# Kernel tuning notes

Measured on AMD Instinct MI355X. Metric: run time of the kernel, lower is better.

Reference implementation:

```python
import jax, jax.numpy as jnp
import numpy as np

IMG_DIM = 256
AUD_DIM = 256
N_HEADS = 8


def _linear_params(key, fan_in, fan_out):
    k1, k2 = jax.random.split(key)
    lim = 1.0 / np.sqrt(fan_in)
    W = jax.random.uniform(k1, (fan_in, fan_out), minval=-lim, maxval=lim, dtype=jnp.float32)
    b = jax.random.uniform(k2, (fan_out,), minval=-lim, maxval=lim, dtype=jnp.float32)
    return W, b


def setup_inputs() -> dict:
    key = jax.random.key(0)
    ks = jax.random.split(key, 16)
    B, Nv, Na = 16, 1024, 512
    inp = {
        "image_feat": jax.random.normal(ks[0], (B, Nv, IMG_DIM), dtype=jnp.float32),
        "audio_feat": jax.random.normal(ks[1], (B, Na, AUD_DIM), dtype=jnp.float32),
    }
    inp["Wq_i"], inp["bq_i"] = _linear_params(ks[2], IMG_DIM, IMG_DIM)
    inp["Wk_i"], inp["bk_i"] = _linear_params(ks[3], IMG_DIM, IMG_DIM)
    inp["Wv_i"], inp["bv_i"] = _linear_params(ks[4], IMG_DIM, IMG_DIM)
    inp["Wo_i"], inp["bo_i"] = _linear_params(ks[5], AUD_DIM, IMG_DIM)  # out_proj_image
    inp["Wq_a"], inp["bq_a"] = _linear_params(ks[6], AUD_DIM, AUD_DIM)
    inp["Wk_a"], inp["bk_a"] = _linear_params(ks[7], AUD_DIM, AUD_DIM)
    inp["Wv_a"], inp["bv_a"] = _linear_params(ks[8], AUD_DIM, AUD_DIM)
    inp["Wo_a"], inp["bo_a"] = _linear_params(ks[9], IMG_DIM, AUD_DIM)  # out_proj_audio
    inp["Wc1_i"], inp["bc1_i"] = _linear_params(ks[10], IMG_DIM + 2, IMG_DIM)
    inp["Wc2_i"], inp["bc2_i"] = _linear_params(ks[11], IMG_DIM, N_HEADS)
    inp["Wc1_a"], inp["bc1_a"] = _linear_params(ks[12], AUD_DIM + 2, AUD_DIM)
    inp["Wc2_a"], inp["bc2_a"] = _linear_params(ks[13], AUD_DIM, N_HEADS)
    inp["Wg_i"], inp["bg_i"] = _linear_params(ks[14], IMG_DIM, IMG_DIM)
    inp["Wg_a"], inp["bg_a"] = _linear_params(ks[15], AUD_DIM, AUD_DIM)
    return inp


def _heads(x, W, b, H):
    # x: [B, N, C] -> [B, H, N, C//H]
    B, N, _ = x.shape
    y = x @ W + b
    return y.reshape(B, N, H, -1).transpose(0, 2, 1, 3)


def _fwd(image_feat, audio_feat,
         Wq_i, bq_i, Wk_i, bk_i, Wv_i, bv_i, Wo_i, bo_i,
         Wq_a, bq_a, Wk_a, bk_a, Wv_a, bv_a, Wo_a, bo_a,
         Wc1_i, bc1_i, Wc2_i, bc2_i, Wc1_a, bc1_a, Wc2_a, bc2_a,
         Wg_i, bg_i, Wg_a, bg_a):
    H = N_HEADS
    B, Nv, Ci = image_feat.shape
    _, Na, Ca = audio_feat.shape
    scale_img = (Ci // H) ** (-0.5)
    scale_aud = (Ca // H) ** (-0.5)

    tp_img = image_feat.mean(axis=1)  # [B, Ci]
    tp_aud = audio_feat.mean(axis=1)  # [B, Ca]
    spatial_cond = jnp.linalg.norm(image_feat, axis=-1).mean(axis=1, keepdims=True)  # [B,1]
    time_cond = jnp.linalg.norm(audio_feat, axis=-1).mean(axis=1, keepdims=True)     # [B,1]

    # --- audio queries attend over image keys/values ---
    Q_a = _heads(audio_feat, Wq_a, bq_a, H)   # [B,H,Na,d]
    K_i = _heads(image_feat, Wk_i, bk_i, H)   # [B,H,Nv,d]
    V_i = _heads(image_feat, Wv_i, bv_i, H)   # [B,H,Nv,d]
    cond_aud = jnp.concatenate([tp_aud, spatial_cond, time_cond], axis=-1)  # [B,Ca+2]
    bias_a = (jax.nn.relu(cond_aud @ Wc1_a + bc1_a) @ Wc2_a + bc2_a)        # [B,H]
    logits_a = jnp.einsum('bhqd,bhkd->bhqk', Q_a, K_i) * scale_aud + bias_a[:, :, None, None]
    attn_a = jax.nn.softmax(logits_a, axis=-1)
    fused_a = jnp.einsum('bhqk,bhkd->bhqd', attn_a, V_i)  # [B,H,Na,d]
    fused_a = fused_a.transpose(0, 2, 1, 3).reshape(B, Na, Ci)
    fused_a = fused_a @ Wo_a + bo_a                        # [B,Na,Ca]
    gate_a = jax.nn.sigmoid(tp_aud @ Wg_a + bg_a)[:, None, :]
    audio_out = gate_a * fused_a + (1.0 - gate_a) * audio_feat

    # --- image queries attend over UPDATED audio keys/values ---
    Q_i = _heads(image_feat, Wq_i, bq_i, H)   # [B,H,Nv,d]
    K_a = _heads(audio_out, Wk_a, bk_a, H)    # [B,H,Na,d]
    V_a = _heads(audio_out, Wv_a, bv_a, H)    # [B,H,Na,d]
    cond_img = jnp.concatenate([tp_img, spatial_cond, time_cond], axis=-1)  # [B,Ci+2]
    bias_i = (jax.nn.relu(cond_img @ Wc1_i + bc1_i) @ Wc2_i + bc2_i)        # [B,H]
    logits_i = jnp.einsum('bhqd,bhkd->bhqk', Q_i, K_a) * scale_img + bias_i[:, :, None, None]
    attn_i = jax.nn.softmax(logits_i, axis=-1)
    fused_i = jnp.einsum('bhqk,bhkd->bhqd', attn_i, V_a)  # [B,H,Nv,d]
    fused_i = fused_i.transpose(0, 2, 1, 3).reshape(B, Nv, Ca)
    fused_i = fused_i @ Wo_i + bo_i                        # [B,Nv,Ci]
    gate_i = jax.nn.sigmoid(tp_img @ Wg_i + bg_i)[:, None, :]
    image_out = gate_i * fused_i + (1.0 - gate_i) * image_feat

    return image_out, audio_out


def reference(image_feat, audio_feat,
              Wq_i, bq_i, Wk_i, bk_i, Wv_i, bv_i, Wo_i, bo_i,
              Wq_a, bq_a, Wk_a, bk_a, Wv_a, bv_a, Wo_a, bo_a,
              Wc1_i, bc1_i, Wc2_i, bc2_i, Wc1_a, bc1_a, Wc2_a, bc2_a,
              Wg_i, bg_i, Wg_a, bg_a):
    return _fwd(image_feat, audio_feat,
                Wq_i, bq_i, Wk_i, bk_i, Wv_i, bv_i, Wo_i, bo_i,
                Wq_a, bq_a, Wk_a, bk_a, Wv_a, bv_a, Wo_a, bo_a,
                Wc1_i, bc1_i, Wc2_i, bc2_i, Wc1_a, bc1_a, Wc2_a, bc2_a,
                Wg_i, bg_i, Wg_a, bg_a)
```

## Files before the change

### kernel.cpp

```cpp
#include <hip/hip_runtime.h>

#define C 256

typedef short s16x8 __attribute__((ext_vector_type(8)));
typedef float f32x4 __attribute__((ext_vector_type(4)));

#if __has_builtin(__builtin_amdgcn_exp2f)
#define EXP2F __builtin_amdgcn_exp2f
#else
#define EXP2F exp2f
#endif

__device__ __forceinline__ unsigned short f2b(float f) {
    unsigned u = __float_as_uint(f);
    unsigned r = (u + 0x7fffu + ((u >> 16) & 1u)) >> 16;
    return (unsigned short)r;
}

__device__ __forceinline__ unsigned pack2(float a, float b) {
    return __builtin_amdgcn_perm(__float_as_uint(b) + 0x8000u,
                                 __float_as_uint(a) + 0x8000u, 0x07060302u);
}

struct WPtrs { const float* src[8]; unsigned short* dst[8]; };

__device__ __forceinline__ void cast_mean_body(
    const float* __restrict__ x, unsigned short* __restrict__ y, float* __restrict__ part,
    int N, int nseg, int b, int seg, int tid) {
    __shared__ float red[4][C];
    int cg = tid & 63, rg = tid >> 6;
    int iters = nseg >> 2;
    const float* xp = x + ((size_t)b * N + (size_t)seg * nseg + rg) * C + cg * 4;
    unsigned short* yp = y + ((size_t)b * N + (size_t)seg * nseg + rg) * C + cg * 4;
    float s0 = 0.f, s1 = 0.f, s2 = 0.f, s3 = 0.f;
    for (int i = 0; i < iters; ++i) {
        float4 v = *(const float4*)(xp + (size_t)i * 4 * C);
        s0 += v.x; s1 += v.y; s2 += v.z; s3 += v.w;
        ushort4 o; o.x = f2b(v.x); o.y = f2b(v.y); o.z = f2b(v.z); o.w = f2b(v.w);
        *(ushort4*)(yp + (size_t)i * 4 * C) = o;
    }
    float4 s4 = {s0, s1, s2, s3};
    *(float4*)&red[rg][cg * 4] = s4;
    __syncthreads();
    float s = red[0][tid] + red[1][tid] + red[2][tid] + red[3][tid];
    part[(b * 8 + seg) * C + tid] = s;
}

__global__ void prep_kernel(const float* __restrict__ img, const float* __restrict__ aud,
                            unsigned short* __restrict__ R1, unsigned short* __restrict__ R4,
                            float* __restrict__ partI, float* __restrict__ partA, WPtrs wp) {
    int x = blockIdx.x, tid = threadIdx.x;
    if (x < 128) {
        cast_mean_body(img, R1, partI, 1024, 128, x >> 3, x & 7, tid);
    } else if (x < 256) {
        int id = x - 128;
        cast_mean_body(aud, R4, partA, 512, 64, id >> 3, id & 7, tid);
    } else {
        int id = x - 256;
        const float* W = wp.src[id >> 2];
        unsigned short* Wt = wp.dst[id >> 2];
        int n = (id & 3) * 64 + (tid & 63);
        int k0 = (tid >> 6) * 64;
#pragma unroll
        for (int kk = 0; kk < 64; kk += 4) {
            float a0 = W[(size_t)(k0 + kk + 0) * C + n];
            float a1 = W[(size_t)(k0 + kk + 1) * C + n];
            float a2 = W[(size_t)(k0 + kk + 2) * C + n];
            float a3 = W[(size_t)(k0 + kk + 3) * C + n];
            ushort4 o; o.x = f2b(a0); o.y = f2b(a1); o.z = f2b(a2); o.w = f2b(a3);
            *(ushort4*)(Wt + (size_t)n * C + k0 + kk) = o;
        }
    }
}

struct GDesc {
    const unsigned short* A;
    const unsigned short* Bt;
    const float* bias;
    unsigned short* Yh;
    int N;
    int start;
    int lnb;
    int bias_on_m;
    float oscale;
};
struct GArgs {
    GDesc d[4];
    int off1, off2, off3;
    int gemm_total;
    const float* partI; const float* partA;
    const float* WgI; const float* WgA;
    const float* bgI; const float* bgA;
    float* gI; float* gA;
    float invNv, invNa;
};

__global__ __launch_bounds__(256, 2) void gemm_multi(GArgs ga) {
    __shared__ unsigned short sA[128 * 40];
    __shared__ unsigned short sB[64 * 40];
    const int bid = blockIdx.x;
    const int tid = threadIdx.x;

    if (bid >= ga.gemm_total) {
        float* t = (float*)sA;
        int id = bid - ga.gemm_total;
        int b = id >> 1, which = id & 1;
        const float* part = which ? ga.partA : ga.partI;
        const float* Wg = which ? ga.WgA : ga.WgI;
        const float* bg = which ? ga.bgA : ga.bgI;
        float* g = which ? ga.gA : ga.gI;
        float invN = which ? ga.invNa : ga.invNv;
        float s = 0.f;
#pragma unroll
        for (int j = 0; j < 8; ++j) s += part[(b * 8 + j) * C + tid];
        t[tid] = s * invN;
        __syncthreads();
        float acc = bg[tid];
#pragma unroll 8
        for (int k = 0; k < C; ++k) acc += t[k] * Wg[k * C + tid];
        g[b * C + tid] = 1.f / (1.f + __expf(-acc));
        return;
    }

    const int j = (bid >= ga.off1) + (bid >= ga.off2) + (bid >= ga.off3);
    const GDesc d = ga.d[j];
    const int local = bid - d.start;
    const int bn = (local & ((1 << d.lnb) - 1)) * 64;
    const int bm = (local >> d.lnb) * 128;

    const int wave = tid >> 6, lane = tid & 63;
    const int quad = lane >> 4, l16 = lane & 15;
    const int ar0 = tid >> 2, ac0 = tid & 3;
    const int ar1 = (tid + 256) >> 2;
    const int br = tid >> 2, bc = tid & 3;

    f32x4 acc[2][4];
#pragma unroll
    for (int i = 0; i < 2; ++i)
#pragma unroll
        for (int k = 0; k < 4; ++k) acc[i][k] = (f32x4){0.f, 0.f, 0.f, 0.f};

    uint4 pa0 = *(const uint4*)(d.A + (size_t)(bm + ar0) * 256 + ac0 * 8);
    uint4 pa1 = *(const uint4*)(d.A + (size_t)(bm + ar1) * 256 + ac0 * 8);
    uint4 pb  = *(const uint4*)(d.Bt + (size_t)(bn + br) * 256 + bc * 8);

    for (int k0 = 0; k0 < 256; k0 += 32) {
        __syncthreads();
        *(uint4*)(sA + ar0 * 40 + ac0 * 8) = pa0;
        *(uint4*)(sA + ar1 * 40 + ac0 * 8) = pa1;
        *(uint4*)(sB + br * 40 + bc * 8) = pb;
        if (k0 < 224) {
            pa0 = *(const uint4*)(d.A + (size_t)(bm + ar0) * 256 + k0 + 32 + ac0 * 8);
            pa1 = *(const uint4*)(d.A + (size_t)(bm + ar1) * 256 + k0 + 32 + ac0 * 8);
            pb  = *(const uint4*)(d.Bt + (size_t)(bn + br) * 256 + k0 + 32 + bc * 8);
        }
        __syncthreads();
        s16x8 af[2], bf[4];
#pragma unroll
        for (int mt = 0; mt < 2; ++mt)
            af[mt] = *(const s16x8*)(sA + (wave * 32 + mt * 16 + l16) * 40 + quad * 8);
#pragma unroll
        for (int nt = 0; nt < 4; ++nt)
            bf[nt] = *(const s16x8*)(sB + (nt * 16 + l16) * 40 + quad * 8);
#pragma unroll
        for (int mt = 0; mt < 2; ++mt)
#pragma unroll
            for (int nt = 0; nt < 4; ++nt)
                acc[mt][nt] = __builtin_amdgcn_mfma_f32_16x16x32_bf16(af[mt], bf[nt], acc[mt][nt], 0, 0, 0);
    }

#pragma unroll
    for (int mt = 0; mt < 2; ++mt) {
#pragma unroll
        for (int nt = 0; nt < 4; ++nt) {
            int n = bn + nt * 16 + l16;
            float bias_n = d.bias_on_m ? 0.f : d.bias[n];
#pragma unroll
            for (int r = 0; r < 4; ++r) {
                int m = bm + wave * 32 + mt * 16 + quad * 4 + r;
                float y = acc[mt][nt][r] + (d.bias_on_m ? d.bias[m] : bias_n);
                d.Yh[(size_t)m * d.N + n] = f2b(y * d.oscale);
            }
        }
    }
}

template <bool STORE_BF16>
__global__ __launch_bounds__(256, 2) void gemm_out(
    const unsigned short* __restrict__ A, const unsigned short* __restrict__ Bt,
    const float* __restrict__ bias, float* __restrict__ Yf, unsigned short* __restrict__ Yh,
    int M, const float* __restrict__ gate, const float* __restrict__ resid, int rows_per_b) {
    __shared__ unsigned short sA[128 * 40];
    __shared__ unsigned short sB[64 * 40];
    const int tid = threadIdx.x;
    const int wave = tid >> 6, lane = tid & 63;
    const int quad = lane >> 4, l16 = lane & 15;
    const int bm = blockIdx.y * 128, bn = blockIdx.x * 64;
    const int ar0 = tid >> 2, ac0 = tid & 3;
    const int ar1 = (tid + 256) >> 2;
    const int br = tid >> 2, bc = tid & 3;

    f32x4 acc[2][4];
#pragma unroll
    for (int i = 0; i < 2; ++i)
#pragma unroll
        for (int k = 0; k < 4; ++k) acc[i][k] = (f32x4){0.f, 0.f, 0.f, 0.f};

    uint4 pa0 = *(const uint4*)(A + (size_t)(bm + ar0) * 256 + ac0 * 8);
    uint4 pa1 = *(const uint4*)(A + (size_t)(bm + ar1) * 256 + ac0 * 8);
    uint4 pb  = *(const uint4*)(Bt + (size_t)(bn + br) * 256 + bc * 8);

    for (int k0 = 0; k0 < 256; k0 += 32) {
        __syncthreads();
        *(uint4*)(sA + ar0 * 40 + ac0 * 8) = pa0;
        *(uint4*)(sA + ar1 * 40 + ac0 * 8) = pa1;
        *(uint4*)(sB + br * 40 + bc * 8) = pb;
        if (k0 < 224) {
            pa0 = *(const uint4*)(A + (size_t)(bm + ar0) * 256 + k0 + 32 + ac0 * 8);
            pa1 = *(const uint4*)(A + (size_t)(bm + ar1) * 256 + k0 + 32 + ac0 * 8);
            pb  = *(const uint4*)(Bt + (size_t)(bn + br) * 256 + k0 + 32 + bc * 8);
        }
        __syncthreads();
        s16x8 af[2], bf[4];
#pragma unroll
        for (int mt = 0; mt < 2; ++mt)
            af[mt] = *(const s16x8*)(sA + (wave * 32 + mt * 16 + l16) * 40 + quad * 8);
#pragma unroll
        for (int nt = 0; nt < 4; ++nt)
            bf[nt] = *(const s16x8*)(sB + (nt * 16 + l16) * 40 + quad * 8);
#pragma unroll
        for (int mt = 0; mt < 2; ++mt)
#pragma unroll
            for (int nt = 0; nt < 4; ++nt)
                acc[mt][nt] = __builtin_amdgcn_mfma_f32_16x16x32_bf16(af[mt], bf[nt], acc[mt][nt], 0, 0, 0);
    }

    const int b = bm / rows_per_b;
#pragma unroll
    for (int mt = 0; mt < 2; ++mt) {
#pragma unroll
        for (int nt = 0; nt < 4; ++nt) {
            int n = bn + nt * 16 + l16;
            float bias_n = bias[n];
            float g = gate[b * C + n];
#pragma unroll
            for (int r = 0; r < 4; ++r) {
                int m = bm + wave * 32 + mt * 16 + quad * 4 + r;
                float y = acc[mt][nt][r] + bias_n;
                float rv = resid[(size_t)m * C + n];
                y = g * y + (1.f - g) * rv;
                Yf[(size_t)m * C + n] = y;
                if (STORE_BF16) Yh[(size_t)m * C + n] = f2b(y);
            }
        }
    }
}

template <int Q2>
__global__ __launch_bounds__(256) void attn_mfma(
    const unsigned short* __restrict__ Q, const unsigned short* __restrict__ K,
    const unsigned short* __restrict__ Vt, unsigned short* __restrict__ O,
    int Nq, int Nk, int vtStride, int lnxb) {
    __shared__ unsigned short sK[64 * 40];
    __shared__ unsigned short sVt[32 * 72];
    __shared__ unsigned short sP[4][Q2][16 * 40];
    const int tid = threadIdx.x;
    const int wave = tid >> 6, lane = tid & 63;
    const int quad = lane >> 4, l16 = lane & 15;
    const int id = blockIdx.x;
    const int slot = id >> 3;
    const int bh = (id & 7) + 8 * (slot >> lnxb);
    const int xb = slot & ((1 << lnxb) - 1);
    const int b = bh >> 3, h = bh & 7;
    const int q0 = xb * (64 * Q2) + wave * (16 * Q2);

    s16x8 qf[Q2];
    f32x4 oacc[Q2][2];
    float rs[Q2];
#pragma unroll
    for (int q = 0; q < Q2; ++q) {
        qf[q] = *(const s16x8*)(Q + ((size_t)b * Nq + q0 + q * 16 + l16) * 256 + h * 32 + quad * 8);
        oacc[q][0] = (f32x4){0.f, 0.f, 0.f, 0.f};
        oacc[q][1] = (f32x4){0.f, 0.f, 0.f, 0.f};
        rs[q] = 0.f;
    }

    const int kr = tid >> 2, kc = tid & 3;
    const int vr = tid >> 3, vc = tid & 7;
    const unsigned short* Kb = K + (size_t)b * Nk * 256 + h * 32;
    const unsigned short* Vb = Vt + (size_t)(h * 32 + vr) * vtStride + (size_t)b * Nk;

    uint4 ka = *(const uint4*)(Kb + (size_t)kr * 256 + kc * 8);
    uint4 va = *(const uint4*)(Vb + vc * 8);
    const int n1 = (64 < Nk) ? 64 : 0;
    uint4 kb = *(const uint4*)(Kb + (size_t)(n1 + kr) * 256 + kc * 8);
    uint4 vb = *(const uint4*)(Vb + n1 + vc * 8);

    for (int k0 = 0; k0 < Nk; k0 += 64) {
        __syncthreads();
        *(uint4*)(sK + kr * 40 + kc * 8) = ka;
        *(uint4*)(sVt + vr * 72 + vc * 8) = va;
        ka = kb; va = vb;
        int np = k0 + 128; if (np >= Nk) np = Nk - 64;
        kb = *(const uint4*)(Kb + (size_t)(np + kr) * 256 + kc * 8);
        vb = *(const uint4*)(Vb + np + vc * 8);
        __syncthreads();

#pragma unroll
        for (int kt = 0; kt < 4; ++kt) {
            s16x8 kf = *(const s16x8*)(sK + (kt * 16 + l16) * 40 + quad * 8);
#pragma unroll
            for (int q = 0; q < Q2; ++q) {
                f32x4 z = (f32x4){0.f, 0.f, 0.f, 0.f};
                f32x4 st = __builtin_amdgcn_mfma_f32_16x16x32_bf16(kf, qf[q], z, 0, 0, 0);
                float p0 = EXP2F(st[0]), p1 = EXP2F(st[1]);
                float p2 = EXP2F(st[2]), p3 = EXP2F(st[3]);
                rs[q] += (p0 + p1) + (p2 + p3);
                uint2 pk;
                pk.x = pack2(p0, p1);
                pk.y = pack2(p2, p3);
                *(uint2*)(&sP[wave][q][0] + l16 * 40 + kt * 16 + quad * 4) = pk;
            }
        }
#pragma unroll
        for (int kg = 0; kg < 2; ++kg) {
            s16x8 vf0 = *(const s16x8*)(sVt + l16 * 72 + kg * 32 + quad * 8);
            s16x8 vf1 = *(const s16x8*)(sVt + (16 + l16) * 72 + kg * 32 + quad * 8);
#pragma unroll
            for (int q = 0; q < Q2; ++q) {
                s16x8 pf = *(const s16x8*)(&sP[wave][q][0] + l16 * 40 + kg * 32 + quad * 8);
                oacc[q][0] = __builtin_amdgcn_mfma_f32_16x16x32_bf16(pf, vf0, oacc[q][0], 0, 0, 0);
                oacc[q][1] = __builtin_amdgcn_mfma_f32_16x16x32_bf16(pf, vf1, oacc[q][1], 0, 0, 0);
            }
        }
    }

#pragma unroll
    for (int q = 0; q < Q2; ++q) {
        float r = rs[q];
        r += __shfl_xor(r, 16, 64);
        r += __shfl_xor(r, 32, 64);
        float inv = 1.f / r;
#pragma unroll
        for (int rr = 0; rr < 4; ++rr) {
            float iq = __shfl(inv, quad * 4 + rr, 64);
#pragma unroll
            for (int dh = 0; dh < 2; ++dh)
                O[((size_t)b * Nq + q0 + q * 16 + quad * 4 + rr) * 256 + h * 32 + dh * 16 + l16] =
                    f2b(oacc[q][dh][rr] * iq);
        }
    }
}

extern "C" void kernel_launch(void* const* d_in, const int* in_sizes, int n_in,
                              void* d_out, int out_size, void* d_ws, size_t ws_size,
                              hipStream_t stream) {
    (void)in_sizes; (void)n_in; (void)out_size; (void)ws_size;
    const float* img  = (const float*)d_in[0];
    const float* aud  = (const float*)d_in[1];
    const float* Wq_i = (const float*)d_in[2];  const float* bq_i = (const float*)d_in[3];
    const float* Wk_i = (const float*)d_in[4];  const float* bk_i = (const float*)d_in[5];
    const float* Wv_i = (const float*)d_in[6];  const float* bv_i = (const float*)d_in[7];
    const float* Wo_i = (const float*)d_in[8];  const float* bo_i = (const float*)d_in[9];
    const float* Wq_a = (const float*)d_in[10]; const float* bq_a = (const float*)d_in[11];
    const float* Wk_a = (const float*)d_in[12]; const float* bk_a = (const float*)d_in[13];
    const float* Wv_a = (const float*)d_in[14]; const float* bv_a = (const float*)d_in[15];
    const float* Wo_a = (const float*)d_in[16]; const float* bo_a = (const float*)d_in[17];
    const float* Wg_i = (const float*)d_in[26]; const float* bg_i = (const float*)d_in[27];
    const float* Wg_a = (const float*)d_in[28]; const float* bg_a = (const float*)d_in[29];

    const int B = 16, Nv = 1024, Na = 512;
    const int Mi = B * Nv, Ma = B * Na;
    const size_t MiC = (size_t)Mi * C;
    const size_t MaC = (size_t)Ma * C;

    float* out_img = (float*)d_out;
    float* out_aud = out_img + MiC;

    unsigned short* wsu = (unsigned short*)d_ws;
    unsigned short* R1 = wsu;
    unsigned short* R2 = R1 + MiC;
    unsigned short* R3 = R2 + MiC;
    unsigned short* R8 = R3 + MiC;
    unsigned short* R4 = R8 + MiC;
    unsigned short* R5 = R4 + MaC;
    unsigned short* R6 = R5 + MaC;
    unsigned short* R7 = R6 + MaC;
    unsigned short* wt = R7 + MaC;
    float* fws   = (float*)(wt + 8 * 65536);
    float* partI = fws;
    float* partA = partI + B * 8 * C;
    float* gI    = partA + B * 8 * C;
    float* gA    = gI + B * C;

    unsigned short* wtQa = wt + 0 * 65536;
    unsigned short* wtKi = wt + 1 * 65536;
    unsigned short* wtVi = wt + 2 * 65536;
    unsigned short* wtOa = wt + 3 * 65536;
    unsigned short* wtKa = wt + 4 * 65536;
    unsigned short* wtVa = wt + 5 * 65536;
    unsigned short* wtQi = wt + 6 * 65536;
    unsigned short* wtOi = wt + 7 * 65536;

    const float qs = 0.17677669529663687f * 1.4426950408889634f;
    dim3 blk(256);

    WPtrs wp;
    wp.src[0] = Wq_a; wp.dst[0] = wtQa;
    wp.src[1] = Wk_i; wp.dst[1] = wtKi;
    wp.src[2] = Wv_i; wp.dst[2] = wtVi;
    wp.src[3] = Wo_a; wp.dst[3] = wtOa;
    wp.src[4] = Wk_a; wp.dst[4] = wtKa;
    wp.src[5] = Wv_a; wp.dst[5] = wtVa;
    wp.src[6] = Wq_i; wp.dst[6] = wtQi;
    wp.src[7] = Wo_i; wp.dst[7] = wtOi;
    prep_kernel<<<288, blk, 0, stream>>>(img, aud, R1, R4, partI, partA, wp);

    GArgs g1 = {};
    g1.d[0] = {R4,   wtQa, bq_a, R5, 256,   0,    2, 0, qs };
    g1.d[1] = {R1,   wtKi, bk_i, R2, 256,   256,  2, 0, 1.f};
    g1.d[2] = {wtVi, R1,   bv_i, R3, 16384, 768,  8, 1, 1.f};
    g1.d[3] = {R1,   wtQi, bq_i, R8, 256,   1280, 2, 0, qs };
    g1.off1 = 256; g1.off2 = 768; g1.off3 = 1280; g1.gemm_total = 1792;
    g1.partI = partI; g1.partA = partA;
    g1.WgI = Wg_i; g1.WgA = Wg_a; g1.bgI = bg_i; g1.bgA = bg_a;
    g1.gI = gI; g1.gA = gA; g1.invNv = 1.f / Nv; g1.invNa = 1.f / Na;
    gemm_multi<<<1792 + 32, blk, 0, stream>>>(g1);

    attn_mfma<2><<<128 * (Na / 128), blk, 0, stream>>>(R5, R2, R3, R6, Na, Nv, Mi, 2);

    gemm_out<true><<<dim3(4, Ma / 128), blk, 0, stream>>>(R6, wtOa, bo_a, out_aud, R7, Ma, gA, aud, Na);

    GArgs g2 = {};
    g2.d[0] = {R7,   wtKa, bk_a, R5, 256,  0,   2, 0, 1.f};
    g2.d[1] = {wtVa, R7,   bv_a, R6, 8192, 256, 7, 1, 1.f};
    g2.off1 = 256; g2.off2 = 512; g2.off3 = 512; g2.gemm_total = 512;
    gemm_multi<<<512, blk, 0, stream>>>(g2);

    attn_mfma<2><<<128 * (Nv / 128), blk, 0, stream>>>(R8, R5, R6, R2, Nv, Na, Ma, 3);

    gemm_out<false><<<dim3(4, Mi / 128), blk, 0, stream>>>(R2, wtOi, bo_i, out_img, nullptr, Mi, gI, img, Nv);
}
```

Measured before the change: 243.9 us.

## Double GEMM K-tile to 64 and interleave attention P-compute with PV per key group

Both GEMM kernels now stage 64-wide K slices in shared memory (row stride 72) with four A and two B vector loads per thread. This halves the number of k-iterations and barrier pairs, at the cost of more LDS and more prefetch registers. The attention kernel now computes softmax probabilities for one 32-key group and immediately runs the PV MFMAs on that group. This lets the per-wave P scratch hold only 32 columns and shortens the gap between producing and consuming P.

New measurement: 319.0 us. 30.8% more time.

```diff
diff --git a/kernel.cpp b/kernel.cpp
--- a/kernel.cpp
+++ b/kernel.cpp
@@ -96,8 +96,8 @@
 };
 
 __global__ __launch_bounds__(256, 2) void gemm_multi(GArgs ga) {
-    __shared__ unsigned short sA[128 * 40];
-    __shared__ unsigned short sB[64 * 40];
+    __shared__ unsigned short sA[128 * 72];
+    __shared__ unsigned short sB[64 * 72];
     const int bid = blockIdx.x;
     const int tid = threadIdx.x;
 
@@ -130,9 +130,11 @@
 
     const int wave = tid >> 6, lane = tid & 63;
     const int quad = lane >> 4, l16 = lane & 15;
-    const int ar0 = tid >> 2, ac0 = tid & 3;
-    const int ar1 = (tid + 256) >> 2;
-    const int br = tid >> 2, bc = tid & 3;
+    int arw[4], acg[4], brw[2], bcg[2];
+#pragma unroll
+    for (int s = 0; s < 4; ++s) { int slot = tid + s * 256; arw[s] = slot >> 3; acg[s] = slot & 7; }
+#pragma unroll
+    for (int s = 0; s < 2; ++s) { int slot = tid + s * 256; brw[s] = slot >> 3; bcg[s] = slot & 7; }
 
     f32x4 acc[2][4];
 #pragma unroll
@@ -140,33 +142,42 @@
 #pragma unroll
         for (int k = 0; k < 4; ++k) acc[i][k] = (f32x4){0.f, 0.f, 0.f, 0.f};
 
-    uint4 pa0 = *(const uint4*)(d.A + (size_t)(bm + ar0) * 256 + ac0 * 8);
-    uint4 pa1 = *(const uint4*)(d.A + (size_t)(bm + ar1) * 256 + ac0 * 8);
-    uint4 pb  = *(const uint4*)(d.Bt + (size_t)(bn + br) * 256 + bc * 8);
-
-    for (int k0 = 0; k0 < 256; k0 += 32) {
-        __syncthreads();
-        *(uint4*)(sA + ar0 * 40 + ac0 * 8) = pa0;
-        *(uint4*)(sA + ar1 * 40 + ac0 * 8) = pa1;
-        *(uint4*)(sB + br * 40 + bc * 8) = pb;
-        if (k0 < 224) {
-            pa0 = *(const uint4*)(d.A + (size_t)(bm + ar0) * 256 + k0 + 32 + ac0 * 8);
-            pa1 = *(const uint4*)(d.A + (size_t)(bm + ar1) * 256 + k0 + 32 + ac0 * 8);
-            pb  = *(const uint4*)(d.Bt + (size_t)(bn + br) * 256 + k0 + 32 + bc * 8);
-        }
-        __syncthreads();
-        s16x8 af[2], bf[4];
-#pragma unroll
-        for (int mt = 0; mt < 2; ++mt)
-            af[mt] = *(const s16x8*)(sA + (wave * 32 + mt * 16 + l16) * 40 + quad * 8);
-#pragma unroll
-        for (int nt = 0; nt < 4; ++nt)
-            bf[nt] = *(const s16x8*)(sB + (nt * 16 + l16) * 40 + quad * 8);
-#pragma unroll
-        for (int mt = 0; mt < 2; ++mt)
+    uint4 pa[4], pb[2];
+#pragma unroll
+    for (int s = 0; s < 4; ++s) pa[s] = *(const uint4*)(d.A + (size_t)(bm + arw[s]) * 256 + acg[s] * 8);
+#pragma unroll
+    for (int s = 0; s < 2; ++s) pb[s] = *(const uint4*)(d.Bt + (size_t)(bn + brw[s]) * 256 + bcg[s] * 8);
+
+    for (int k0 = 0; k0 < 256; k0 += 64) {
+        __syncthreads();
+#pragma unroll
+        for (int s = 0; s < 4; ++s) *(uint4*)(sA + arw[s] * 72 + acg[s] * 8) = pa[s];
+#pragma unroll
+        for (int s = 0; s < 2; ++s) *(uint4*)(sB + brw[s] * 72 + bcg[s] * 8) = pb[s];
+        if (k0 < 192) {
+#pragma unroll
+            for (int s = 0; s < 4; ++s)
+                pa[s] = *(const uint4*)(d.A + (size_t)(bm + arw[s]) * 256 + k0 + 64 + acg[s] * 8);
+#pragma unroll
+            for (int s = 0; s < 2; ++s)
+                pb[s] = *(const uint4*)(d.Bt + (size_t)(bn + brw[s]) * 256 + k0 + 64 + bcg[s] * 8);
+        }
+        __syncthreads();
+#pragma unroll
+        for (int ks = 0; ks < 2; ++ks) {
+            s16x8 af[2], bf[4];
+#pragma unroll
+            for (int mt = 0; mt < 2; ++mt)
+                af[mt] = *(const s16x8*)(sA + (wave * 32 + mt * 16 + l16) * 72 + ks * 32 + quad * 8);
 #pragma unroll
             for (int nt = 0; nt < 4; ++nt)
-                acc[mt][nt] = __builtin_amdgcn_mfma_f32_16x16x32_bf16(af[mt], bf[nt], acc[mt][nt], 0, 0, 0);
+                bf[nt] = *(const s16x8*)(sB + (nt * 16 + l16) * 72 + ks * 32 + quad * 8);
+#pragma unroll
+            for (int mt = 0; mt < 2; ++mt)
+#pragma unroll
+                for (int nt = 0; nt < 4; ++nt)
+                    acc[mt][nt] = __builtin_amdgcn_mfma_f32_16x16x32_bf16(af[mt], bf[nt], acc[mt][nt], 0, 0, 0);
+        }
     }
 
 #pragma unroll
@@ -190,15 +201,17 @@
     const unsigned short* __restrict__ A, const unsigned short* __restrict__ Bt,
     const float* __restrict__ bias, float* __restrict__ Yf, unsigned short* __restrict__ Yh,
     int M, const float* __restrict__ gate, const float* __restrict__ resid, int rows_per_b) {
-    __shared__ unsigned short sA[128 * 40];
-    __shared__ unsigned short sB[64 * 40];
+    __shared__ unsigned short sA[128 * 72];
+    __shared__ unsigned short sB[64 * 72];
     const int tid = threadIdx.x;
     const int wave = tid >> 6, lane = tid & 63;
     const int quad = lane >> 4, l16 = lane & 15;
     const int bm = blockIdx.y * 128, bn = blockIdx.x * 64;
-    const int ar0 = tid >> 2, ac0 = tid & 3;
-    const int ar1 = (tid + 256) >> 2;
-    const int br = tid >> 2, bc = tid & 3;
+    int arw[4], acg[4], brw[2], bcg[2];
+#pragma unroll
+    for (int s = 0; s < 4; ++s) { int slot = tid + s * 256; arw[s] = slot >> 3; acg[s] = slot & 7; }
+#pragma unroll
+    for (int s = 0; s < 2; ++s) { int slot = tid + s * 256; brw[s] = slot >> 3; bcg[s] = slot & 7; }
 
     f32x4 acc[2][4];
 #pragma unroll
@@ -206,33 +219,42 @@
 #pragma unroll
         for (int k = 0; k < 4; ++k) acc[i][k] = (f32x4){0.f, 0.f, 0.f, 0.f};
 
-    uint4 pa0 = *(const uint4*)(A + (size_t)(bm + ar0) * 256 + ac0 * 8);
-    uint4 pa1 = *(const uint4*)(A + (size_t)(bm + ar1) * 256 + ac0 * 8);
-    uint4 pb  = *(const uint4*)(Bt + (size_t)(bn + br) * 256 + bc * 8);
-
-    for (int k0 = 0; k0 < 256; k0 += 32) {
-        __syncthreads();
-        *(uint4*)(sA + ar0 * 40 + ac0 * 8) = pa0;
-        *(uint4*)(sA + ar1 * 40 + ac0 * 8) = pa1;
-        *(uint4*)(sB + br * 40 + bc * 8) = pb;
-        if (k0 < 224) {
-            pa0 = *(const uint4*)(A + (size_t)(bm + ar0) * 256 + k0 + 32 + ac0 * 8);
-            pa1 = *(const uint4*)(A + (size_t)(bm + ar1) * 256 + k0 + 32 + ac0 * 8);
-            pb  = *(const uint4*)(Bt + (size_t)(bn + br) * 256 + k0 + 32 + bc * 8);
-        }
-        __syncthreads();
-        s16x8 af[2], bf[4];
-#pragma unroll
-        for (int mt = 0; mt < 2; ++mt)
-            af[mt] = *(const s16x8*)(sA + (wave * 32 + mt * 16 + l16) * 40 + quad * 8);
-#pragma unroll
-        for (int nt = 0; nt < 4; ++nt)
-            bf[nt] = *(const s16x8*)(sB + (nt * 16 + l16) * 40 + quad * 8);
-#pragma unroll
-        for (int mt = 0; mt < 2; ++mt)
+    uint4 pa[4], pb[2];
+#pragma unroll
+    for (int s = 0; s < 4; ++s) pa[s] = *(const uint4*)(A + (size_t)(bm + arw[s]) * 256 + acg[s] * 8);
+#pragma unroll
+    for (int s = 0; s < 2; ++s) pb[s] = *(const uint4*)(Bt + (size_t)(bn + brw[s]) * 256 + bcg[s] * 8);
+
+    for (int k0 = 0; k0 < 256; k0 += 64) {
+        __syncthreads();
+#pragma unroll
+        for (int s = 0; s < 4; ++s) *(uint4*)(sA + arw[s] * 72 + acg[s] * 8) = pa[s];
+#pragma unroll
+        for (int s = 0; s < 2; ++s) *(uint4*)(sB + brw[s] * 72 + bcg[s] * 8) = pb[s];
+        if (k0 < 192) {
+#pragma unroll
+            for (int s = 0; s < 4; ++s)
+                pa[s] = *(const uint4*)(A + (size_t)(bm + arw[s]) * 256 + k0 + 64 + acg[s] * 8);
+#pragma unroll
+            for (int s = 0; s < 2; ++s)
+                pb[s] = *(const uint4*)(Bt + (size_t)(bn + brw[s]) * 256 + k0 + 64 + bcg[s] * 8);
+        }
+        __syncthreads();
+#pragma unroll
+        for (int ks = 0; ks < 2; ++ks) {
+            s16x8 af[2], bf[4];
+#pragma unroll
+            for (int mt = 0; mt < 2; ++mt)
+                af[mt] = *(const s16x8*)(sA + (wave * 32 + mt * 16 + l16) * 72 + ks * 32 + quad * 8);
 #pragma unroll
             for (int nt = 0; nt < 4; ++nt)
-                acc[mt][nt] = __builtin_amdgcn_mfma_f32_16x16x32_bf16(af[mt], bf[nt], acc[mt][nt], 0, 0, 0);
+                bf[nt] = *(const s16x8*)(sB + (nt * 16 + l16) * 72 + ks * 32 + quad * 8);
+#pragma unroll
+            for (int mt = 0; mt < 2; ++mt)
+#pragma unroll
+                for (int nt = 0; nt < 4; ++nt)
+                    acc[mt][nt] = __builtin_amdgcn_mfma_f32_16x16x32_bf16(af[mt], bf[nt], acc[mt][nt], 0, 0, 0);
+        }
     }
 
     const int b = bm / rows_per_b;
@@ -307,28 +329,28 @@
         __syncthreads();
 
 #pragma unroll
-        for (int kt = 0; kt < 4; ++kt) {
-            s16x8 kf = *(const s16x8*)(sK + (kt * 16 + l16) * 40 + quad * 8);
-#pragma unroll
-            for (int q = 0; q < Q2; ++q) {
-                f32x4 z = (f32x4){0.f, 0.f, 0.f, 0.f};
-                f32x4 st = __builtin_amdgcn_mfma_f32_16x16x32_bf16(kf, qf[q], z, 0, 0, 0);
-                float p0 = EXP2F(st[0]), p1 = EXP2F(st[1]);
-                float p2 = EXP2F(st[2]), p3 = EXP2F(st[3]);
-                rs[q] += (p0 + p1) + (p2 + p3);
-                uint2 pk;
-                pk.x = pack2(p0, p1);
-                pk.y = pack2(p2, p3);
-                *(uint2*)(&sP[wave][q][0] + l16 * 40 + kt * 16 + quad * 4) = pk;
+        for (int kg = 0; kg < 2; ++kg) {
+#pragma unroll
+            for (int kt = 0; kt < 2; ++kt) {
+                s16x8 kf = *(const s16x8*)(sK + (kg * 32 + kt * 16 + l16) * 40 + quad * 8);
+#pragma unroll
+                for (int q = 0; q < Q2; ++q) {
+                    f32x4 z = (f32x4){0.f, 0.f, 0.f, 0.f};
+                    f32x4 st = __builtin_amdgcn_mfma_f32_16x16x32_bf16(kf, qf[q], z, 0, 0, 0);
+                    float p0 = EXP2F(st[0]), p1 = EXP2F(st[1]);
+                    float p2 = EXP2F(st[2]), p3 = EXP2F(st[3]);
+                    rs[q] += (p0 + p1) + (p2 + p3);
+                    uint2 pk;
+                    pk.x = pack2(p0, p1);
+                    pk.y = pack2(p2, p3);
+                    *(uint2*)(&sP[wave][q][0] + l16 * 40 + kt * 16 + quad * 4) = pk;
+                }
             }
-        }
-#pragma unroll
-        for (int kg = 0; kg < 2; ++kg) {
             s16x8 vf0 = *(const s16x8*)(sVt + l16 * 72 + kg * 32 + quad * 8);
             s16x8 vf1 = *(const s16x8*)(sVt + (16 + l16) * 72 + kg * 32 + quad * 8);
 #pragma unroll
             for (int q = 0; q < Q2; ++q) {
-                s16x8 pf = *(const s16x8*)(&sP[wave][q][0] + l16 * 40 + kg * 32 + quad * 8);
+                s16x8 pf = *(const s16x8*)(&sP[wave][q][0] + l16 * 40 + quad * 8);
                 oacc[q][0] = __builtin_amdgcn_mfma_f32_16x16x32_bf16(pf, vf0, oacc[q][0], 0, 0, 0);
                 oacc[q][1] = __builtin_amdgcn_mfma_f32_16x16x32_bf16(pf, vf1, oacc[q][1], 0, 0, 0);
             }
```
